# Performance work log

Hardware: AMD Instinct MI355X
Metric: run time of the kernel (lower is better)

## Reference

```python
import jax, jax.numpy as jnp
import numpy as np

N, E = 100000, 1600000
IN, OUT = 64, 64
R, B = 16, 4
EPS = 1e-5


def setup_inputs() -> dict:
    key = jax.random.key(0)
    ks = jax.random.split(key, 8)
    s_in = 1.0 / np.sqrt(IN)
    return {
        "node_feat": jax.random.normal(ks[0], (N, IN), jnp.float32),
        "bases": jax.random.normal(ks[1], (B, IN, OUT), jnp.float32) * s_in,
        "comp": jax.random.normal(ks[2], (R, B), jnp.float32) * (1.0 / np.sqrt(B)),
        "loop_weight": jax.random.normal(ks[3], (IN, OUT), jnp.float32) * s_in,
        "bias": jnp.zeros((OUT,), jnp.float32),
        "gamma": jnp.ones((OUT,), jnp.float32),
        "beta": jnp.zeros((OUT,), jnp.float32),
        "src": jax.random.randint(ks[4], (E,), 0, N, jnp.int32),
        "dst": jax.random.randint(ks[5], (E,), 0, N, jnp.int32),
        "edge_types": jax.random.randint(ks[6], (E,), 0, R, jnp.int32),
    }


def reference(node_feat, bases, comp, loop_weight, bias, gamma, beta, src, dst, edge_types):
    n = node_feat.shape[0]
    # basis decomposition: W_r = sum_b comp[r,b] * V_b  -> [R, in, out]
    W = jnp.einsum('rb,bio->rio', comp, bases)
    # per-node, per-relation transform (avoids [E,in,out] per-edge weight gather)
    h_all = jnp.einsum('ni,rio->nro', node_feat, W)        # [N, R, out]
    m = h_all[src, edge_types]                             # [E, out] per-edge messages
    agg = jax.ops.segment_sum(m, dst, num_segments=n)      # scatter-add to dst
    out = agg + node_feat @ loop_weight + bias             # self-loop + bias (DGL defaults)
    out = jnp.where(out >= 0, out, 0.1 * out)              # LeakyReLU(0.1)
    mu = jnp.mean(out, axis=-1, keepdims=True)
    var = jnp.mean(jnp.square(out - mu), axis=-1, keepdims=True)
    return (out - mu) * jax.lax.rsqrt(var + EPS) * gamma + beta
```

## Files before the change

### kernel.cpp

```cpp
#include <hip/hip_runtime.h>

#define N_NODES 100000
#define N_EDGES 1600000
#define NBINS   100000
#define LN_EPS  1e-5f

#define NG 8
#define NS 32
#define RANGE 12500
#define SLICE_I4 12500
#define SCAN_BLOCKS 98

#define XB_BLOCKS   64
#define AGG_BLOCKS  2048
#define NPW 13

typedef unsigned int u32;
typedef unsigned short u16;
typedef __attribute__((ext_vector_type(8))) short short8;
typedef __attribute__((ext_vector_type(4))) float f32x4;

__device__ __forceinline__ u16 f2bf(float f) {
    u32 u = __float_as_uint(f);
    u32 r = (u + 0x7FFFu + ((u >> 16) & 1u)) >> 16;
    return (u16)r;
}
__device__ __forceinline__ float bf2f(u16 h) {
    return __uint_as_float((u32)h << 16);
}

__global__ __launch_bounds__(1024) void k_prep_hist(
    const float* __restrict__ x, const float* __restrict__ bases,
    const float* __restrict__ loopw, const int* __restrict__ dst,
    u16* __restrict__ wf, u16* __restrict__ xb, u32* __restrict__ priv)
{
    __shared__ u32 lh[RANGE];
    const int t = threadIdx.x;
    if (blockIdx.x < NG * NS) {
        for (int j = t; j < RANGE; j += 1024) lh[j] = 0u;
        __syncthreads();
        const int s = blockIdx.x & (NS - 1);
        const int g = blockIdx.x >> 5;
        const int lo = g * RANGE;
        const int4* dst4 = (const int4*)dst;
        const int i0 = s * SLICE_I4;
        for (int i = i0 + t; i < i0 + SLICE_I4; i += 1024) {
            const int4 d4 = dst4[i];
#pragma unroll
            for (int q = 0; q < 4; ++q) {
                const int d = (q == 0) ? d4.x : (q == 1) ? d4.y
                            : (q == 2) ? d4.z : d4.w;
                const u32 rel = (u32)(d - lo);
                if (rel < (u32)RANGE) atomicAdd(&lh[rel], 1u);
            }
        }
        __syncthreads();
        u32* pb = priv + (size_t)(g * NS + s) * RANGE;
        for (int j = t; j < RANGE; j += 1024) pb[j] = lh[j];
    } else if (blockIdx.x == NG * NS) {
        for (int idx = t; idx < 4 * 10 * 64 * 8; idx += 1024) {
            const int j = idx & 7;
            const int l = (idx >> 3) & 63;
            const int rest = idx >> 9;
            const int ks = rest % 10;
            const int ct = rest / 10;
            const int k = ks * 32 + (l >> 4) * 8 + j;
            const int c = ct * 16 + (l & 15);
            float v;
            if (k < 256) v = bases[(k & 3) * 4096 + (k >> 2) * 64 + c];
            else         v = loopw[(k - 256) * 64 + c];
            wf[idx] = f2bf(v);
        }
    } else {
        const int bb = blockIdx.x - NG * NS - 1;
        for (int i = bb * 1024 + t; i < N_NODES * 16; i += XB_BLOCKS * 1024) {
            const float4 v = ((const float4*)x)[i];
            uint2 w;
            w.x = (u32)f2bf(v.x) | ((u32)f2bf(v.y) << 16);
            w.y = (u32)f2bf(v.z) | ((u32)f2bf(v.w) << 16);
            ((uint2*)xb)[i] = w;
        }
    }
}

__global__ __launch_bounds__(1024) void k_scan_block(
    u32* __restrict__ priv, u32* __restrict__ counts,
    u32* __restrict__ offs, u32* __restrict__ bsums)
{
    __shared__ u32 wsum[16];
    const int t = threadIdx.x;
    const int lane = t & 63, wid = t >> 6;
    const int idx = blockIdx.x * 1024 + t;
    u32 sv[NS];
    u32 v = 0u;
    u32 g = 0, local = 0;
    if (idx < NBINS) {
        g = (u32)idx / (u32)RANGE;
        local = (u32)idx - g * (u32)RANGE;
#pragma unroll
        for (int s = 0; s < NS; ++s) {
            sv[s] = priv[(size_t)(g * NS + s) * RANGE + local];
            v += sv[s];
        }
    }
    u32 sc = v;
#pragma unroll
    for (int off = 1; off < 64; off <<= 1) {
        u32 u = __shfl_up(sc, off, 64);
        if (lane >= off) sc += u;
    }
    if (lane == 63) wsum[wid] = sc;
    __syncthreads();
    if (wid == 0) {
        u32 w = (lane < 16) ? wsum[lane] : 0u;
#pragma unroll
        for (int off = 1; off < 16; off <<= 1) {
            u32 u = __shfl_up(w, off, 64);
            if (lane >= off) w += u;
        }
        if (lane < 16) wsum[lane] = w;
    }
    __syncthreads();
    const u32 prefix = (wid > 0) ? wsum[wid - 1] : 0u;
    const u32 incl = sc + prefix;
    const u32 excl = incl - v;
    if (idx < NBINS) {
        offs[idx] = excl;
        counts[idx] = v;
        u32 run = excl;
#pragma unroll
        for (int s = 0; s < NS; ++s) {
            priv[(size_t)(g * NS + s) * RANGE + local] = run;
            run += sv[s];
        }
    }
    if (t == 1023) bsums[blockIdx.x] = incl;
}

__global__ __launch_bounds__(1024) void k_scatter(
    const int* __restrict__ dst, const int* __restrict__ src,
    const int* __restrict__ et,
    const u32* __restrict__ priv, const u32* __restrict__ bsums,
    u32* __restrict__ boffs, u32* __restrict__ packed)
{
    __shared__ u32 cur[RANGE];
    __shared__ u32 sb[128];
    const int t = threadIdx.x;
    if (t < 64) {
        const u32 a = (t < SCAN_BLOCKS) ? bsums[t] : 0u;
        u32 s1 = a;
#pragma unroll
        for (int off = 1; off < 64; off <<= 1) {
            u32 u = __shfl_up(s1, off, 64);
            if (t >= off) s1 += u;
        }
        sb[t] = s1 - a;
        const u32 tot0 = __shfl(s1, 63, 64);
        const int t2 = t + 64;
        const u32 b = (t2 < SCAN_BLOCKS) ? bsums[t2] : 0u;
        u32 s2 = b;
#pragma unroll
        for (int off = 1; off < 64; off <<= 1) {
            u32 u = __shfl_up(s2, off, 64);
            if (t >= off) s2 += u;
        }
        sb[t2] = tot0 + s2 - b;
    }
    __syncthreads();

    const int s = blockIdx.x & (NS - 1);
    const int g = blockIdx.x >> 5;
    const int lo = g * RANGE;
    if (blockIdx.x == 0) {
        if (t < 128) boffs[t] = sb[t];
    }
    const u32* pb = priv + (size_t)(g * NS + s) * RANGE;
    for (int j = t; j < RANGE; j += 1024)
        cur[j] = pb[j] + sb[(lo + j) >> 10];
    __syncthreads();
    const int4* dst4 = (const int4*)dst;
    const int4* src4 = (const int4*)src;
    const int4* et4  = (const int4*)et;
    const int i0 = s * SLICE_I4;
    for (int i = i0 + t; i < i0 + SLICE_I4; i += 1024) {
        const int4 d4 = dst4[i];
        const int4 s4 = src4[i];
        const int4 e4 = et4[i];
#pragma unroll
        for (int q = 0; q < 4; ++q) {
            const int d = (q == 0) ? d4.x : (q == 1) ? d4.y
                        : (q == 2) ? d4.z : d4.w;
            const int sn = (q == 0) ? s4.x : (q == 1) ? s4.y
                         : (q == 2) ? s4.z : s4.w;
            const int ev = (q == 0) ? e4.x : (q == 1) ? e4.y
                         : (q == 2) ? e4.z : e4.w;
            const u32 rel = (u32)(d - lo);
            if (rel < (u32)RANGE) {
                const u32 pos = atomicAdd(&cur[rel], 1u);
                packed[pos] = (u32)sn | ((u32)ev << 20);
            }
        }
    }
}

__global__ __launch_bounds__(256) void k_agg(
    const u16* __restrict__ xb, const float4* __restrict__ comp,
    const u32* __restrict__ packed,
    const u32* __restrict__ offs, const u32* __restrict__ boffs,
    const u32* __restrict__ counts,
    uint2* __restrict__ y)
{
    const int t = threadIdx.x;
    const int lane = t & 63;
    const int wid = t >> 6;
    const u16* xbl = xb + lane;

    int w = blockIdx.x * 4 + wid;
    w = __builtin_amdgcn_readfirstlane(w);
    int n = w * NPW;
    if (n >= N_NODES) return;
    const int nEnd = (n + NPW < N_NODES) ? n + NPW : N_NODES;

    const u32 base = offs[n] + boffs[n >> 10];
    const u32 end  = (nEnd < N_NODES) ? offs[nEnd] + boffs[nEnd >> 10]
                                      : (u32)N_EDGES;
    const u32 total = end - base;

    float a0 = 0.f, a1 = 0.f, a2 = 0.f, a3 = 0.f;
    u32 r = 0;
    while (n < nEnd) {
        r = counts[n];
        if (r) break;
        y[(size_t)n * 64 + lane] = (uint2){0u, 0u};
        ++n;
    }

    u32 idx0 = base + (u32)lane;
    if (idx0 > (u32)(N_EDGES - 1)) idx0 = (u32)(N_EDGES - 1);
    u32 recs = packed[idx0];

    u32 done = 0;
    while (done < total) {
        u32 cnt = total - done;
        if (cnt > 64u) cnt = 64u;
        const u32 nd = done + cnt;
        u32 recs_next = 0u;
        if (nd < total) {
            u32 idx = base + nd + (u32)lane;
            if (idx > (u32)(N_EDGES - 1)) idx = (u32)(N_EDGES - 1);
            recs_next = packed[idx];
        }
        u32 k = 0;
        while (k < cnt) {
            if (r == 0u) break;
            u32 m = (r < cnt - k) ? r : (cnt - k);
            const u32 kend = k + m;
            for (; k + 8 <= kend; k += 8) {
                u32 rr[8];
#pragma unroll
                for (int q = 0; q < 8; ++q)
                    rr[q] = (u32)__builtin_amdgcn_readlane((int)recs, (int)(k + q));
                u16 hv[8];
#pragma unroll
                for (int q = 0; q < 8; ++q)
                    hv[q] = xbl[(size_t)(rr[q] & 0xFFFFFu) * 64];
                float4 cc[8];
#pragma unroll
                for (int q = 0; q < 8; ++q) cc[q] = comp[rr[q] >> 20];
#pragma unroll
                for (int q = 0; q < 8; ++q) {
                    const float xf = bf2f(hv[q]);
                    a0 = fmaf(cc[q].x, xf, a0);
                    a1 = fmaf(cc[q].y, xf, a1);
                    a2 = fmaf(cc[q].z, xf, a2);
                    a3 = fmaf(cc[q].w, xf, a3);
                }
            }
            for (; k < kend; ++k) {
                const u32 r0 = (u32)__builtin_amdgcn_readlane((int)recs, (int)k);
                const float4 c0 = comp[r0 >> 20];
                const float xf = bf2f(xbl[(size_t)(r0 & 0xFFFFFu) * 64]);
                a0 = fmaf(c0.x, xf, a0);
                a1 = fmaf(c0.y, xf, a1);
                a2 = fmaf(c0.z, xf, a2);
                a3 = fmaf(c0.w, xf, a3);
            }
            r -= m;
            if (r == 0u) {
                uint2 wv;
                wv.x = (u32)f2bf(a0) | ((u32)f2bf(a1) << 16);
                wv.y = (u32)f2bf(a2) | ((u32)f2bf(a3) << 16);
                y[(size_t)n * 64 + lane] = wv;
                a0 = a1 = a2 = a3 = 0.f;
                ++n;
                while (n < nEnd) {
                    r = counts[n];
                    if (r) break;
                    y[(size_t)n * 64 + lane] = (uint2){0u, 0u};
                    ++n;
                }
            }
        }
        done = nd;
        recs = recs_next;
    }
}

__global__ __launch_bounds__(256) void k_gemm_ln(
    const short8* __restrict__ yf,
    const short8* __restrict__ xbf,
    const short8* __restrict__ wf,
    const float* __restrict__ bias, const float* __restrict__ gamma,
    const float* __restrict__ beta, float* __restrict__ out)
{
    const int lane = threadIdx.x & 63;
    const int wid = threadIdx.x >> 6;
    const int m = lane & 15, kg = lane >> 4;
    float bsv[4], gm[4], bt[4];
#pragma unroll
    for (int ct = 0; ct < 4; ++ct) {
        bsv[ct] = bias[ct * 16 + m];
        gm[ct] = gamma[ct * 16 + m];
        bt[ct] = beta[ct * 16 + m];
    }
    const int ntiles = N_NODES / 16;
    for (int tile = blockIdx.x * 4 + wid; tile < ntiles; tile += gridDim.x * 4) {
        const int base = tile * 16;
        const int row = base + m;
        short8 a[10];
#pragma unroll
        for (int ks = 0; ks < 8; ++ks)
            a[ks] = yf[(size_t)row * 32 + ks * 4 + kg];
        a[8] = xbf[(size_t)row * 8 + kg];
        a[9] = xbf[(size_t)row * 8 + 4 + kg];
        f32x4 acc[4];
#pragma unroll
        for (int ct = 0; ct < 4; ++ct) {
            acc[ct] = (f32x4){0.f, 0.f, 0.f, 0.f};
#pragma unroll
            for (int ks = 0; ks < 10; ++ks)
                acc[ct] = __builtin_amdgcn_mfma_f32_16x16x32_bf16(
                    a[ks], wf[(ct * 10 + ks) * 64 + lane], acc[ct], 0, 0, 0);
        }
        float v[4][4];
#pragma unroll
        for (int ct = 0; ct < 4; ++ct)
#pragma unroll
            for (int r = 0; r < 4; ++r) {
                const float u = acc[ct][r] + bsv[ct];
                v[ct][r] = (u >= 0.f) ? u : 0.1f * u;
            }
#pragma unroll
        for (int r = 0; r < 4; ++r) {
            float s1 = v[0][r] + v[1][r] + v[2][r] + v[3][r];
#pragma unroll
            for (int mk = 1; mk < 16; mk <<= 1) s1 += __shfl_xor(s1, mk, 64);
            const float mu = s1 * (1.f / 64.f);
            float s2 = 0.f;
#pragma unroll
            for (int ct = 0; ct < 4; ++ct) {
                const float d = v[ct][r] - mu;
                s2 += d * d;
            }
#pragma unroll
            for (int mk = 1; mk < 16; mk <<= 1) s2 += __shfl_xor(s2, mk, 64);
            const float rstd = rsqrtf(s2 * (1.f / 64.f) + LN_EPS);
            const int ro = base + kg * 4 + r;
#pragma unroll
            for (int ct = 0; ct < 4; ++ct)
                out[(size_t)ro * 64 + ct * 16 + m] =
                    (v[ct][r] - mu) * rstd * gm[ct] + bt[ct];
        }
    }
}

__global__ __launch_bounds__(256) void k_edge_direct(
    const float* __restrict__ x, const float* __restrict__ bases,
    const float* __restrict__ comp,
    const int* __restrict__ src, const int* __restrict__ dst,
    const int* __restrict__ et, float* __restrict__ agg)
{
    const int lane = threadIdx.x & 63;
    int e = blockIdx.x * 4 + (threadIdx.x >> 6);
    if (e >= N_EDGES) return;
    e = __builtin_amdgcn_readfirstlane(e);
    const int s = src[e], d = dst[e], r = et[e];
    const float4 c = *(const float4*)(comp + r * 4);
    const float* xr = x + (size_t)s * 64;
    float acc = 0.f;
    for (int i = 0; i < 64; ++i) {
        const float w = c.x * bases[i * 64 + lane]
                      + c.y * bases[4096 + i * 64 + lane]
                      + c.z * bases[8192 + i * 64 + lane]
                      + c.w * bases[12288 + i * 64 + lane];
        acc = fmaf(xr[i], w, acc);
    }
    atomicAdd(&agg[(size_t)d * 64 + lane], acc);
}

__global__ __launch_bounds__(256) void k_finalize(
    const float* __restrict__ x, const float* __restrict__ loopw,
    const float* __restrict__ bias, const float* __restrict__ gamma,
    const float* __restrict__ beta, float* __restrict__ out)
{
    const int t = threadIdx.x;
    const int lane = t & 63;
    const int wid = t >> 6;
    float wreg[64];
#pragma unroll
    for (int i = 0; i < 64; ++i)
        wreg[i] = loopw[i * 64 + lane];
    const float bs = bias[lane], gm = gamma[lane], bt = beta[lane];
    const int waves = gridDim.x * 4;
    for (int n = blockIdx.x * 4 + wid; n < N_NODES; n += waves) {
        float xv = x[(size_t)n * 64 + lane];
        const int xbv = __float_as_int(xv);
        float slv = bs;
#pragma unroll
        for (int i = 0; i < 64; ++i) {
            const float s = __int_as_float(__builtin_amdgcn_readlane(xbv, i));
            slv = fmaf(s, wreg[i], slv);
        }
        float v = out[(size_t)n * 64 + lane] + slv;
        v = (v >= 0.f) ? v : 0.1f * v;
        float s1 = v;
#pragma unroll
        for (int mm = 32; mm >= 1; mm >>= 1) s1 += __shfl_xor(s1, mm, 64);
        const float mu = s1 * (1.f / 64.f);
        const float dv = v - mu;
        float s2 = dv * dv;
#pragma unroll
        for (int mm = 32; mm >= 1; mm >>= 1) s2 += __shfl_xor(s2, mm, 64);
        const float var = s2 * (1.f / 64.f);
        out[(size_t)n * 64 + lane] = dv * rsqrtf(var + LN_EPS) * gm + bt;
    }
}

extern "C" void kernel_launch(void* const* d_in, const int* in_sizes, int n_in,
                              void* d_out, int out_size, void* d_ws, size_t ws_size,
                              hipStream_t stream) {
    const float* x     = (const float*)d_in[0];
    const float* bases = (const float*)d_in[1];
    const float* comp  = (const float*)d_in[2];
    const float* loopw = (const float*)d_in[3];
    const float* bias  = (const float*)d_in[4];
    const float* gamma = (const float*)d_in[5];
    const float* beta  = (const float*)d_in[6];
    const int*   src   = (const int*)d_in[7];
    const int*   dst   = (const int*)d_in[8];
    const int*   et    = (const int*)d_in[9];
    float* out = (float*)d_out;

    size_t p = 0;
    auto alloc = [&](size_t bytes) {
        size_t cur = p;
        p = (p + bytes + 255) & ~(size_t)255;
        return cur;
    };
    char* ws = (char*)d_ws;
    const size_t o_counts = alloc((size_t)NBINS * sizeof(u32));
    const size_t o_wf     = alloc((size_t)4 * 10 * 64 * 8 * sizeof(u16));
    const size_t o_xb     = alloc((size_t)N_NODES * 64 * sizeof(u16));
    const size_t o_y      = alloc((size_t)N_NODES * 256 * sizeof(u16));
    const size_t o_priv   = alloc((size_t)NG * NS * RANGE * sizeof(u32));
    const size_t o_offs   = alloc((size_t)NBINS * sizeof(u32));
    const size_t o_bsums  = alloc(128 * sizeof(u32));
    const size_t o_boffs  = alloc(128 * sizeof(u32));
    const size_t o_packed = alloc((size_t)N_EDGES * sizeof(u32));
    const size_t need = p;

    if (ws_size >= need) {
        u32* counts = (u32*)(ws + o_counts);
        u16* wfp    = (u16*)(ws + o_wf);
        u16* xb     = (u16*)(ws + o_xb);
        u16* y      = (u16*)(ws + o_y);
        u32* priv   = (u32*)(ws + o_priv);
        u32* offs   = (u32*)(ws + o_offs);
        u32* bsums  = (u32*)(ws + o_bsums);
        u32* boffs  = (u32*)(ws + o_boffs);
        u32* packed = (u32*)(ws + o_packed);

        k_prep_hist<<<NG * NS + 1 + XB_BLOCKS, 1024, 0, stream>>>(
            x, bases, loopw, dst, wfp, xb, priv);
        k_scan_block<<<SCAN_BLOCKS, 1024, 0, stream>>>(priv, counts, offs, bsums);
        k_scatter<<<NG * NS, 1024, 0, stream>>>(dst, src, et, priv, bsums,
                                                boffs, packed);
        k_agg<<<AGG_BLOCKS, 256, 0, stream>>>(xb, (const float4*)comp, packed,
                                              offs, boffs, counts, (uint2*)y);
        k_gemm_ln<<<(N_NODES / 16 + 3) / 4, 256, 0, stream>>>(
            (const short8*)y, (const short8*)xb, (const short8*)wfp,
            bias, gamma, beta, out);
    } else {
        hipMemsetAsync(d_out, 0, (size_t)N_NODES * 64 * sizeof(float), stream);
        k_edge_direct<<<(N_EDGES + 3) / 4, 256, 0, stream>>>(
            x, bases, comp, src, dst, et, out);
        k_finalize<<<2048, 256, 0, stream>>>(x, loopw, bias, gamma, beta, out);
    }
}
```

Before: 130.2 us.

## Fuse edge aggregation with the GEMM+LayerNorm epilogue through swizzled LDS tiles

Merges the aggregation kernel and the MFMA GEMM/LayerNorm kernel into one. Each wavefront aggregates a 16-node tile into XOR-swizzled shared memory, then loads its MFMA A-operands directly from LDS. This removes the global round trip of the 51 MB intermediate y buffer and one kernel launch. In exchange, each wave now covers 16 nodes instead of 13, giving a different load balance and grid size, and the LDS use may limit occupancy.

```diff
diff --git a/kernel.cpp b/kernel.cpp
--- a/kernel.cpp
+++ b/kernel.cpp
@@ -12,8 +12,6 @@
 #define SCAN_BLOCKS 98
 
 #define XB_BLOCKS   64
-#define AGG_BLOCKS  2048
-#define NPW 13
 
 typedef unsigned int u32;
 typedef unsigned short u16;
@@ -203,13 +201,16 @@
     }
 }
 
-__global__ __launch_bounds__(256) void k_agg(
+__global__ __launch_bounds__(256) void k_agg_gemm_ln(
     const u16* __restrict__ xb, const float4* __restrict__ comp,
     const u32* __restrict__ packed,
     const u32* __restrict__ offs, const u32* __restrict__ boffs,
     const u32* __restrict__ counts,
-    uint2* __restrict__ y)
-{
+    const short8* __restrict__ wf,
+    const float* __restrict__ bias, const float* __restrict__ gamma,
+    const float* __restrict__ beta, float* __restrict__ out)
+{
+    __shared__ uint2 ylds[4][16][64];
     const int t = threadIdx.x;
     const int lane = t & 63;
     const int wid = t >> 6;
@@ -217,21 +218,25 @@
 
     int w = blockIdx.x * 4 + wid;
     w = __builtin_amdgcn_readfirstlane(w);
-    int n = w * NPW;
-    if (n >= N_NODES) return;
-    const int nEnd = (n + NPW < N_NODES) ? n + NPW : N_NODES;
-
-    const u32 base = offs[n] + boffs[n >> 10];
+    const int tileBase = w * 16;
+    if (tileBase >= N_NODES) return;
+    const int nEnd = tileBase + 16;
+
+    uint2* yl = &ylds[wid][0][0];
+
+    const u32 base = offs[tileBase] + boffs[tileBase >> 10];
     const u32 end  = (nEnd < N_NODES) ? offs[nEnd] + boffs[nEnd >> 10]
                                       : (u32)N_EDGES;
     const u32 total = end - base;
 
+    int n = tileBase;
     float a0 = 0.f, a1 = 0.f, a2 = 0.f, a3 = 0.f;
     u32 r = 0;
     while (n < nEnd) {
         r = counts[n];
         if (r) break;
-        y[(size_t)n * 64 + lane] = (uint2){0u, 0u};
+        const int m = n - tileBase;
+        yl[m * 64 + (lane ^ ((m & 7) << 1))] = (uint2){0u, 0u};
         ++n;
     }
 
@@ -287,16 +292,18 @@
             }
             r -= m;
             if (r == 0u) {
+                const int mc = n - tileBase;
                 uint2 wv;
                 wv.x = (u32)f2bf(a0) | ((u32)f2bf(a1) << 16);
                 wv.y = (u32)f2bf(a2) | ((u32)f2bf(a3) << 16);
-                y[(size_t)n * 64 + lane] = wv;
+                yl[mc * 64 + (lane ^ ((mc & 7) << 1))] = wv;
                 a0 = a1 = a2 = a3 = 0.f;
                 ++n;
                 while (n < nEnd) {
                     r = counts[n];
                     if (r) break;
-                    y[(size_t)n * 64 + lane] = (uint2){0u, 0u};
+                    const int m2 = n - tileBase;
+                    yl[m2 * 64 + (lane ^ ((m2 & 7) << 1))] = (uint2){0u, 0u};
                     ++n;
                 }
             }
@@ -304,18 +311,23 @@
         done = nd;
         recs = recs_next;
     }
-}
-
-__global__ __launch_bounds__(256) void k_gemm_ln(
-    const short8* __restrict__ yf,
-    const short8* __restrict__ xbf,
-    const short8* __restrict__ wf,
-    const float* __restrict__ bias, const float* __restrict__ gamma,
-    const float* __restrict__ beta, float* __restrict__ out)
-{
-    const int lane = threadIdx.x & 63;
-    const int wid = threadIdx.x >> 6;
+
     const int m = lane & 15, kg = lane >> 4;
+    const int sw = (m & 7) << 1;
+    const uint4* yrow = (const uint4*)(yl + m * 64);
+    union UA { uint4 q; short8 v; };
+    short8 a[10];
+#pragma unroll
+    for (int ks = 0; ks < 8; ++ks) {
+        const int c = ks * 8 + kg * 2;
+        UA u; u.q = yrow[(c ^ sw) >> 1];
+        a[ks] = u.v;
+    }
+    const short8* xbf = (const short8*)xb;
+    const int row = tileBase + m;
+    a[8] = xbf[(size_t)row * 8 + kg];
+    a[9] = xbf[(size_t)row * 8 + 4 + kg];
+
     float bsv[4], gm[4], bt[4];
 #pragma unroll
     for (int ct = 0; ct < 4; ++ct) {
@@ -323,54 +335,43 @@
         gm[ct] = gamma[ct * 16 + m];
         bt[ct] = beta[ct * 16 + m];
     }
-    const int ntiles = N_NODES / 16;
-    for (int tile = blockIdx.x * 4 + wid; tile < ntiles; tile += gridDim.x * 4) {
-        const int base = tile * 16;
-        const int row = base + m;
-        short8 a[10];
-#pragma unroll
-        for (int ks = 0; ks < 8; ++ks)
-            a[ks] = yf[(size_t)row * 32 + ks * 4 + kg];
-        a[8] = xbf[(size_t)row * 8 + kg];
-        a[9] = xbf[(size_t)row * 8 + 4 + kg];
-        f32x4 acc[4];
+    f32x4 acc[4];
+#pragma unroll
+    for (int ct = 0; ct < 4; ++ct) {
+        acc[ct] = (f32x4){0.f, 0.f, 0.f, 0.f};
+#pragma unroll
+        for (int ks = 0; ks < 10; ++ks)
+            acc[ct] = __builtin_amdgcn_mfma_f32_16x16x32_bf16(
+                a[ks], wf[(ct * 10 + ks) * 64 + lane], acc[ct], 0, 0, 0);
+    }
+    float v[4][4];
+#pragma unroll
+    for (int ct = 0; ct < 4; ++ct)
+#pragma unroll
+        for (int rr = 0; rr < 4; ++rr) {
+            const float u = acc[ct][rr] + bsv[ct];
+            v[ct][rr] = (u >= 0.f) ? u : 0.1f * u;
+        }
+#pragma unroll
+    for (int rr = 0; rr < 4; ++rr) {
+        float s1 = v[0][rr] + v[1][rr] + v[2][rr] + v[3][rr];
+#pragma unroll
+        for (int mk = 1; mk < 16; mk <<= 1) s1 += __shfl_xor(s1, mk, 64);
+        const float mu = s1 * (1.f / 64.f);
+        float s2 = 0.f;
 #pragma unroll
         for (int ct = 0; ct < 4; ++ct) {
-            acc[ct] = (f32x4){0.f, 0.f, 0.f, 0.f};
-#pragma unroll
-            for (int ks = 0; ks < 10; ++ks)
-                acc[ct] = __builtin_amdgcn_mfma_f32_16x16x32_bf16(
-                    a[ks], wf[(ct * 10 + ks) * 64 + lane], acc[ct], 0, 0, 0);
-        }
-        float v[4][4];
+            const float d = v[ct][rr] - mu;
+            s2 += d * d;
+        }
+#pragma unroll
+        for (int mk = 1; mk < 16; mk <<= 1) s2 += __shfl_xor(s2, mk, 64);
+        const float rstd = rsqrtf(s2 * (1.f / 64.f) + LN_EPS);
+        const int ro = tileBase + kg * 4 + rr;
 #pragma unroll
         for (int ct = 0; ct < 4; ++ct)
-#pragma unroll
-            for (int r = 0; r < 4; ++r) {
-                const float u = acc[ct][r] + bsv[ct];
-                v[ct][r] = (u >= 0.f) ? u : 0.1f * u;
-            }
-#pragma unroll
-        for (int r = 0; r < 4; ++r) {
-            float s1 = v[0][r] + v[1][r] + v[2][r] + v[3][r];
-#pragma unroll
-            for (int mk = 1; mk < 16; mk <<= 1) s1 += __shfl_xor(s1, mk, 64);
-            const float mu = s1 * (1.f / 64.f);
-            float s2 = 0.f;
-#pragma unroll
-            for (int ct = 0; ct < 4; ++ct) {
-                const float d = v[ct][r] - mu;
-                s2 += d * d;
-            }
-#pragma unroll
-            for (int mk = 1; mk < 16; mk <<= 1) s2 += __shfl_xor(s2, mk, 64);
-            const float rstd = rsqrtf(s2 * (1.f / 64.f) + LN_EPS);
-            const int ro = base + kg * 4 + r;
-#pragma unroll
-            for (int ct = 0; ct < 4; ++ct)
-                out[(size_t)ro * 64 + ct * 16 + m] =
-                    (v[ct][r] - mu) * rstd * gm[ct] + bt[ct];
-        }
+            out[(size_t)ro * 64 + ct * 16 + m] =
+                (v[ct][rr] - mu) * rstd * gm[ct] + bt[ct];
     }
 }
 
@@ -461,7 +462,6 @@
     const size_t o_counts = alloc((size_t)NBINS * sizeof(u32));
     const size_t o_wf     = alloc((size_t)4 * 10 * 64 * 8 * sizeof(u16));
     const size_t o_xb     = alloc((size_t)N_NODES * 64 * sizeof(u16));
-    const size_t o_y      = alloc((size_t)N_NODES * 256 * sizeof(u16));
     const size_t o_priv   = alloc((size_t)NG * NS * RANGE * sizeof(u32));
     const size_t o_offs   = alloc((size_t)NBINS * sizeof(u32));
     const size_t o_bsums  = alloc(128 * sizeof(u32));
@@ -473,7 +473,6 @@
         u32* counts = (u32*)(ws + o_counts);
         u16* wfp    = (u16*)(ws + o_wf);
         u16* xb     = (u16*)(ws + o_xb);
-        u16* y      = (u16*)(ws + o_y);
         u32* priv   = (u32*)(ws + o_priv);
         u32* offs   = (u32*)(ws + o_offs);
         u32* bsums  = (u32*)(ws + o_bsums);
@@ -485,11 +484,10 @@
         k_scan_block<<<SCAN_BLOCKS, 1024, 0, stream>>>(priv, counts, offs, bsums);
         k_scatter<<<NG * NS, 1024, 0, stream>>>(dst, src, et, priv, bsums,
                                                 boffs, packed);
-        k_agg<<<AGG_BLOCKS, 256, 0, stream>>>(xb, (const float4*)comp, packed,
-                                              offs, boffs, counts, (uint2*)y);
-        k_gemm_ln<<<(N_NODES / 16 + 3) / 4, 256, 0, stream>>>(
-            (const short8*)y, (const short8*)xb, (const short8*)wfp,
-            bias, gamma, beta, out);
+        const int tiles = N_NODES / 16;
+        k_agg_gemm_ln<<<(tiles + 3) / 4, 256, 0, stream>>>(
+            xb, (const float4*)comp, packed, offs, boffs, counts,
+            (const short8*)wfp, bias, gamma, beta, out);
     } else {
         hipMemsetAsync(d_out, 0, (size_t)N_NODES * 64 * sizeof(float), stream);
         k_edge_direct<<<(N_EDGES + 3) / 4, 256, 0, stream>>>(
```

After: 149.5 us. +14.8%, slower.
